# Kernel tuning notes

Measured on AMD Instinct MI355X. Metric: run time of the kernel, lower is better.

Reference implementation:

```python
import jax, jax.numpy as jnp
import numpy as np

B, T, C = 2, 2048, 2048
NH, NKV = 16, 4
HD = C // NH  # 128


def _rope(x, cos, sin):
    d = x.shape[-1] // 2
    x1, x2 = x[..., :d], x[..., d:]
    return jnp.concatenate([x1 * cos + x2 * sin, -x1 * sin + x2 * cos], axis=-1)


def _rmsnorm(x):
    eps = jnp.finfo(x.dtype).eps
    return x * jax.lax.rsqrt(jnp.mean(jnp.square(x), axis=-1, keepdims=True) + eps)


def setup_inputs() -> dict:
    key = jax.random.key(0)
    ks = jax.random.split(key, 7)
    s = 0.02
    return {
        "x": jax.random.normal(ks[0], (B, T, C), jnp.float32),
        "cos": jax.random.normal(ks[1], (1, T, 1, HD // 2), jnp.float32),
        "sin": jax.random.normal(ks[2], (1, T, 1, HD // 2), jnp.float32),
        "wq": jax.random.normal(ks[3], (C, NH * HD), jnp.float32) * s,
        "wk": jax.random.normal(ks[4], (C, NKV * HD), jnp.float32) * s,
        "wv": jax.random.normal(ks[5], (C, NKV * HD), jnp.float32) * s,
        "wo": jax.random.normal(ks[6], (C, C), jnp.float32) * s,
    }


def reference(x, cos, sin, wq, wk, wv, wo):
    q = (x @ wq).reshape(B, T, NH, HD)
    k = (x @ wk).reshape(B, T, NKV, HD)
    v = (x @ wv).reshape(B, T, NKV, HD)
    q = _rmsnorm(_rope(q, cos, sin))
    k = _rmsnorm(_rope(k, cos, sin))
    # [B, H, T, D]
    q = q.transpose(0, 2, 1, 3)
    k = k.transpose(0, 2, 1, 3)
    v = v.transpose(0, 2, 1, 3)
    rep = NH // NKV
    k = jnp.repeat(k, rep, axis=1)
    v = jnp.repeat(v, rep, axis=1)
    scale = 1.0 / jnp.sqrt(jnp.float32(HD))
    scores = jnp.einsum("bhqd,bhkd->bhqk", q, k) * scale
    causal = jnp.tril(jnp.ones((T, T), bool))
    scores = jnp.where(causal, scores, jnp.finfo(scores.dtype).min)
    attn = jax.nn.softmax(scores, axis=-1)
    y = jnp.einsum("bhqk,bhkd->bhqd", attn, v)
    y = y.transpose(0, 2, 1, 3).reshape(B, T, C)
    return y @ wo
```

## Files before the change

### kernel.cpp

```cpp
#include <hip/hip_runtime.h>
#include <hip/hip_bf16.h>
#include <cstdint>

typedef unsigned short u16;
typedef __bf16 bf16x8 __attribute__((ext_vector_type(8)));
typedef float f32x4 __attribute__((ext_vector_type(4)));
typedef unsigned short u16x4 __attribute__((ext_vector_type(4)));
typedef unsigned uint2v __attribute__((ext_vector_type(2)));

#define B_ 2
#define T_ 2048
#define C_ 2048
#define NH_ 16
#define NKV_ 4
#define HD_ 128
#define K2_ 0.12752004650581538f

__device__ __forceinline__ u16 f2bf(float f) {
    unsigned u = __builtin_bit_cast(unsigned, f);
    unsigned r = u + 0x7FFFu + ((u >> 16) & 1u);
    return (u16)(r >> 16);
}

__device__ __forceinline__ unsigned cvtpk(float a, float b) {
    unsigned r;
    asm("v_cvt_pk_bf16_f32 %0, %1, %2" : "=v"(r) : "v"(a), "v"(b));
    return r;
}

__device__ __forceinline__ void gl16(const void* g, void* l) {
    auto gp = reinterpret_cast<const __attribute__((address_space(1))) unsigned*>(
        reinterpret_cast<uintptr_t>(g));
    auto lp = reinterpret_cast<__attribute__((address_space(3))) unsigned*>(
        reinterpret_cast<uintptr_t>(l));
    __builtin_amdgcn_global_load_lds(gp, lp, 16, 0, 0);
}

__global__ void transpose_conv(const float* __restrict__ in, u16* __restrict__ out, int N) {
    __shared__ float tile[32][33];
    int n0 = blockIdx.x * 32, k0 = blockIdx.y * 32;
    int tx = threadIdx.x, ty = threadIdx.y;
#pragma unroll
    for (int i = 0; i < 4; ++i)
        tile[ty * 4 + i][tx] = in[(size_t)(k0 + ty * 4 + i) * N + n0 + tx];
    __syncthreads();
#pragma unroll
    for (int i = 0; i < 4; ++i)
        out[(size_t)(n0 + ty * 4 + i) * 2048 + k0 + tx] = f2bf(tile[tx][ty * 4 + i]);
}

__global__ void convert4(const float4* __restrict__ in, u16* __restrict__ out) {
    int i = blockIdx.x * 256 + threadIdx.x;
    float4 v = in[i];
    u16x4 o;
    o[0] = f2bf(v.x); o[1] = f2bf(v.y); o[2] = f2bf(v.z); o[3] = f2bf(v.w);
    ((u16x4*)out)[i] = o;
}

__global__ __launch_bounds__(256, 2) void gemm_bf16(const u16* __restrict__ A,
                                                    const u16* __restrict__ BT,
                                                    float* __restrict__ C, int N, int K) {
    __shared__ __align__(16) u16 As[128 * 64];
    __shared__ __align__(16) u16 Bs[128 * 64];
    int nwg = gridDim.x * gridDim.y;
    int bid = blockIdx.y * gridDim.x + blockIdx.x;
    int nb = (bid & 7) * (nwg >> 3) + (bid >> 3);
    int bx = nb % gridDim.x, by = nb / gridDim.x;

    int t = threadIdx.x;
    int w = t >> 6, l = t & 63;
    int wr = w >> 1, wc = w & 1;
    int lg = l >> 4, lr = l & 15;
    int m0 = by * 128, n0 = bx * 128;
    f32x4 acc[4][4] = {};
    int ar = t >> 3;
    int acb = (t & 7) * 16;
    const char* Abase = (const char*)(A + (size_t)(m0 + ar) * K) + acb;
    const char* Bbase = (const char*)(BT + (size_t)(n0 + ar) * K) + acb;
    char* AsB = (char*)As + t * 16;
    char* BsB = (char*)Bs + t * 16;
    for (int kt = 0; kt < K; kt += 64) {
        if (kt) __syncthreads();
#pragma unroll
        for (int i = 0; i < 4; ++i) {
            gl16(Abase + (size_t)(i * 32) * K * 2 + (size_t)kt * 2, AsB + i * 4096);
            gl16(Bbase + (size_t)(i * 32) * K * 2 + (size_t)kt * 2, BsB + i * 4096);
        }
        __syncthreads();
#pragma unroll
        for (int kk = 0; kk < 2; ++kk) {
            bf16x8 af[4], bfr[4];
#pragma unroll
            for (int m = 0; m < 4; ++m)
                af[m] = *(const bf16x8*)(As + (wr * 64 + m * 16 + lr) * 64 + kk * 32 + lg * 8);
#pragma unroll
            for (int n = 0; n < 4; ++n)
                bfr[n] = *(const bf16x8*)(Bs + (wc * 64 + n * 16 + lr) * 64 + kk * 32 + lg * 8);
#pragma unroll
            for (int m = 0; m < 4; ++m)
#pragma unroll
                for (int n = 0; n < 4; ++n)
                    acc[m][n] = __builtin_amdgcn_mfma_f32_16x16x32_bf16(af[m], bfr[n], acc[m][n], 0, 0, 0);
        }
    }
#pragma unroll
    for (int m = 0; m < 4; ++m) {
        int row = m0 + wr * 64 + m * 16 + lg * 4;
#pragma unroll
        for (int n = 0; n < 4; ++n) {
            int col = n0 + wc * 64 + n * 16 + lr;
            float* Cp = C + (size_t)row * N + col;
#pragma unroll
            for (int r = 0; r < 4; ++r)
                Cp[(size_t)r * N] = acc[m][n][r];
        }
    }
}

__global__ void rope_rms(const float* __restrict__ qkv, const float* __restrict__ cs,
                         const float* __restrict__ sn, u16* __restrict__ qh,
                         u16* __restrict__ kh) {
    int task = blockIdx.x * 4 + (threadIdx.x >> 6);
    int l = threadIdx.x & 63;
    const float* in;
    u16* out;
    int tpos;
    float post = 1.0f;
    if (task < 65536) {
        int row = task >> 4, h = task & 15;
        in = qkv + (size_t)row * 3072 + h * 128;
        int b = row >> 11; tpos = row & 2047;
        out = qh + ((size_t)(b * NH_ + h) * T_ + tpos) * HD_;
        post = K2_;
    } else {
        int t2 = task - 65536;
        int row = t2 >> 2, h = t2 & 3;
        in = qkv + (size_t)row * 3072 + 2048 + h * 128;
        int b = row >> 11; tpos = row & 2047;
        out = kh + ((size_t)(b * NKV_ + h) * T_ + tpos) * HD_;
    }
    float x1 = in[l], x2 = in[l + 64];
    float c = cs[tpos * 64 + l], s = sn[tpos * 64 + l];
    float o1 = x1 * c + x2 * s;
    float o2 = -x1 * s + x2 * c;
    float ss = o1 * o1 + o2 * o2;
#pragma unroll
    for (int m = 1; m < 64; m <<= 1) ss += __shfl_xor(ss, m);
    float r = rsqrtf(ss * (1.0f / 128.0f) + 1.1920929e-07f) * post;
    out[l] = f2bf(o1 * r);
    out[l + 64] = f2bf(o2 * r);
}

__global__ void transpose_v(const float* __restrict__ qkv, u16* __restrict__ vt) {
    __shared__ float tile[32][33];
    int t0 = blockIdx.x * 32;
    int d0 = blockIdx.y * 32;
    int bk = blockIdx.z;
    int b = bk >> 2, kvh = bk & 3;
    int tx = threadIdx.x, ty = threadIdx.y;
#pragma unroll
    for (int i = 0; i < 4; ++i)
        tile[ty * 4 + i][tx] =
            qkv[(size_t)(b * 2048 + t0 + ty * 4 + i) * 3072 + 2560 + kvh * 128 + d0 + tx];
    __syncthreads();
#pragma unroll
    for (int i = 0; i < 4; ++i)
        vt[((size_t)bk * 128 + d0 + ty * 4 + i) * 2048 + t0 + tx] = f2bf(tile[tx][ty * 4 + i]);
}

__global__ __launch_bounds__(256, 2) void attn(const u16* __restrict__ Q,
                                               const u16* __restrict__ Kk,
                                               const u16* __restrict__ V,
                                               u16* __restrict__ Y) {
    extern __shared__ __align__(16) u16 sm[];
    u16* Ks = sm;
    u16* Vs = sm + 16384;
    u16* Pb = sm + 32768;

    int bid = blockIdx.x;
    int xcd = bid & 7;
    int b = xcd >> 2, kvh = xcd & 3;
    int q = bid >> 3;
    int j = (q < 32) ? (63 - q) : (q - 32);
    int NN = (j >> 1) + 1;
    int t = threadIdx.x;
    int w = t >> 6, l = t & 63;
    int lg = l >> 4, lr = l & 15;
    int h = kvh * 4 + w;
    int qw = j * 32;

    const u16* Qp = Q + (size_t)(b * NH_ + h) * T_ * HD_;
    const u16* Kp = Kk + (size_t)(b * NKV_ + kvh) * T_ * HD_;
    const u16* Vp = V + (size_t)(b * NKV_ + kvh) * HD_ * T_;
    u16* Yp = Y + (size_t)(b * T_) * 2048 + h * HD_;
    u16* Pw = Pb + w * 2048;

    size_t koff[4], voff[4];
#pragma unroll
    for (int i = 0; i < 4; ++i) {
        int g = t + i * 256;
        koff[i] = (size_t)(g >> 4) * 256 + (size_t)(((g & 15) ^ ((g >> 4) & 15)) * 16);
        voff[i] = (size_t)(g >> 3) * (T_ * 2) + (size_t)(((g & 7) ^ ((g >> 3) & 7)) * 16);
    }
    auto stage = [&](int kv0, int buf) {
        const char* Kb = (const char*)Kp + (size_t)kv0 * 256;
        const char* Vb = (const char*)Vp + (size_t)kv0 * 2;
        char* Kd = (char*)Ks + buf * 16384 + t * 16;
        char* Vd = (char*)Vs + buf * 16384 + t * 16;
#pragma unroll
        for (int i = 0; i < 4; ++i) {
            gl16(Kb + koff[i], Kd + i * 4096);
            gl16(Vb + voff[i], Vd + i * 4096);
        }
    };

    bf16x8 aq[2][4];
#pragma unroll
    for (int qf = 0; qf < 2; ++qf)
#pragma unroll
        for (int ch = 0; ch < 4; ++ch)
            aq[qf][ch] = *(const bf16x8*)(Qp + (size_t)(qw + qf * 16 + lr) * HD_ + ch * 32 + lg * 8);

    f32x4 acc[2][8] = {};
    float m2[2] = {-1e30f, -1e30f};
    float lp_[2] = {0.0f, 0.0f};

    stage(0, 0);

    for (int gi = 0; gi < NN; ++gi) {
        asm volatile("s_waitcnt vmcnt(0)" ::: "memory");
        __builtin_amdgcn_s_barrier();
        __builtin_amdgcn_sched_barrier(0);
        int cur = gi & 1;
        if (gi + 1 < NN) stage((gi + 1) * 64, cur ^ 1);
        int kv0 = gi * 64;
        int kbase = cur * 8192;

        f32x4 sc[2][4] = {};
        __builtin_amdgcn_s_setprio(1);
#pragma unroll
        for (int ch = 0; ch < 4; ++ch)
#pragma unroll
            for (int kf = 0; kf < 4; ++kf) {
                bf16x8 bk = *(const bf16x8*)&Ks[kbase + (kf * 16 + lr) * 128 + (((ch * 4 + lg) ^ lr) * 8)];
                sc[0][kf] = __builtin_amdgcn_mfma_f32_16x16x32_bf16(bk, aq[0][ch], sc[0][kf], 0, 0, 0);
                sc[1][kf] = __builtin_amdgcn_mfma_f32_16x16x32_bf16(bk, aq[1][ch], sc[1][kf], 0, 0, 0);
            }
        __builtin_amdgcn_s_setprio(0);

        if (kv0 + 63 > qw) {
#pragma unroll
            for (int qf = 0; qf < 2; ++qf) {
                int qrow = qw + qf * 16 + lr;
#pragma unroll
                for (int kf = 0; kf < 4; ++kf)
#pragma unroll
                    for (int r = 0; r < 4; ++r) {
                        int key = kv0 + kf * 16 + 4 * lg + r;
                        if (key > qrow) sc[qf][kf][r] = -1e38f;
                    }
            }
        }
        float mx[2];
#pragma unroll
        for (int qf = 0; qf < 2; ++qf) {
            float m = sc[qf][0][0];
#pragma unroll
            for (int kf = 0; kf < 4; ++kf)
#pragma unroll
                for (int r = 0; r < 4; ++r) m = fmaxf(m, sc[qf][kf][r]);
            m = fmaxf(m, __shfl_xor(m, 16));
            m = fmaxf(m, __shfl_xor(m, 32));
            mx[qf] = m;
        }
        bool upd = (mx[0] > m2[0] + 8.0f) || (mx[1] > m2[1] + 8.0f);
        if (__any(upd)) {
#pragma unroll
            for (int qf = 0; qf < 2; ++qf) {
                float mn = fmaxf(m2[qf], mx[qf]);
                float rs = exp2f(m2[qf] - mn);
                m2[qf] = mn;
                lp_[qf] *= rs;
                float rs4[4];
#pragma unroll
                for (int r = 0; r < 4; ++r) rs4[r] = __shfl(rs, 4 * lg + r, 16);
#pragma unroll
                for (int oc = 0; oc < 8; ++oc)
#pragma unroll
                    for (int r = 0; r < 4; ++r) acc[qf][oc][r] *= rs4[r];
            }
        }
#pragma unroll
        for (int qf = 0; qf < 2; ++qf) {
            float ps = 0.0f;
#pragma unroll
            for (int kf = 0; kf < 4; ++kf) {
                float p0 = exp2f(sc[qf][kf][0] - m2[qf]);
                float p1 = exp2f(sc[qf][kf][1] - m2[qf]);
                float p2 = exp2f(sc[qf][kf][2] - m2[qf]);
                float p3 = exp2f(sc[qf][kf][3] - m2[qf]);
                ps += (p0 + p1) + (p2 + p3);
                uint2v pk;
                pk[0] = cvtpk(p0, p1);
                pk[1] = cvtpk(p2, p3);
                int g16 = 2 * kf + (lg >> 1);
                *(uint2v*)&Pw[(qf * 16 + lr) * 64 + ((g16 ^ (lr & 7)) * 8) + (lg & 1) * 4] = pk;
            }
            lp_[qf] += ps;
        }
        bf16x8 ap[2][2];
#pragma unroll
        for (int qf = 0; qf < 2; ++qf)
#pragma unroll
            for (int kk = 0; kk < 2; ++kk)
                ap[qf][kk] = *(const bf16x8*)&Pw[(qf * 16 + lr) * 64 + (((4 * kk + lg) ^ (lr & 7)) * 8)];
        __builtin_amdgcn_s_setprio(1);
#pragma unroll
        for (int oc = 0; oc < 8; ++oc)
#pragma unroll
            for (int kk = 0; kk < 2; ++kk) {
                bf16x8 bv = *(const bf16x8*)&Vs[kbase + (oc * 16 + lr) * 64 +
                                                (((kk * 4 + lg) ^ (lr & 7)) * 8)];
                acc[0][oc] = __builtin_amdgcn_mfma_f32_16x16x32_bf16(ap[0][kk], bv, acc[0][oc], 0, 0, 0);
                acc[1][oc] = __builtin_amdgcn_mfma_f32_16x16x32_bf16(ap[1][kk], bv, acc[1][oc], 0, 0, 0);
            }
        __builtin_amdgcn_s_setprio(0);
    }
#pragma unroll
    for (int qf = 0; qf < 2; ++qf) {
        float lt = lp_[qf];
        lt += __shfl_xor(lt, 16);
        lt += __shfl_xor(lt, 32);
        float inv = 1.0f / lt;
        float inv4[4];
#pragma unroll
        for (int r = 0; r < 4; ++r) inv4[r] = __shfl(inv, 4 * lg + r, 16);
#pragma unroll
        for (int oc = 0; oc < 8; ++oc)
#pragma unroll
            for (int r = 0; r < 4; ++r)
                Yp[(size_t)(qw + qf * 16 + 4 * lg + r) * 2048 + oc * 16 + lr] =
                    f2bf(acc[qf][oc][r] * inv4[r]);
    }
}

extern "C" void kernel_launch(void* const* d_in, const int* in_sizes, int n_in,
                              void* d_out, int out_size, void* d_ws, size_t ws_size,
                              hipStream_t stream) {
    const float* x    = (const float*)d_in[0];
    const float* cosT = (const float*)d_in[1];
    const float* sinT = (const float*)d_in[2];
    const float* wq   = (const float*)d_in[3];
    const float* wk   = (const float*)d_in[4];
    const float* wv   = (const float*)d_in[5];
    const float* wo   = (const float*)d_in[6];
    float* out = (float*)d_out;

    char* ws = (char*)d_ws;
    u16*   wqkvT = (u16*)(ws);
    u16*   woT   = (u16*)(ws + 12582912);
    u16*   xb    = (u16*)(ws + 20971520);
    float* qkv   = (float*)(ws + 37748736);
    u16*   qh    = (u16*)(ws + 88080384);
    u16*   kh    = (u16*)(ws + 104857600);
    u16*   vt    = (u16*)(ws + 109051904);
    u16*   y     = xb;

    hipFuncSetAttribute(reinterpret_cast<const void*>(&attn),
                        hipFuncAttributeMaxDynamicSharedMemorySize, 81920);

    transpose_conv<<<dim3(64, 64), dim3(32, 8), 0, stream>>>(wq, wqkvT, 2048);
    transpose_conv<<<dim3(16, 64), dim3(32, 8), 0, stream>>>(wk, wqkvT + (size_t)2048 * 2048, 512);
    transpose_conv<<<dim3(16, 64), dim3(32, 8), 0, stream>>>(wv, wqkvT + (size_t)2560 * 2048, 512);
    transpose_conv<<<dim3(64, 64), dim3(32, 8), 0, stream>>>(wo, woT, 2048);
    convert4<<<8192, 256, 0, stream>>>((const float4*)x, xb);

    gemm_bf16<<<dim3(24, 32), 256, 0, stream>>>(xb, wqkvT, qkv, 3072, 2048);

    rope_rms<<<20480, 256, 0, stream>>>(qkv, cosT, sinT, qh, kh);
    transpose_v<<<dim3(64, 4, 8), dim3(32, 8), 0, stream>>>(qkv, vt);

    attn<<<512, 256, 81920, stream>>>(qh, kh, vt, y);

    gemm_bf16<<<dim3(16, 32), 256, 0, stream>>>(y, woT, out, 2048, 2048);
}
```

Baseline: 224.4 us.

## Double-buffer GEMM LDS tiles with XOR swizzle and halve attention P scratch

The bf16 GEMM now stages the next K tile into a second LDS buffer while the current one feeds MFMAs, using one wait and barrier per iteration instead of two syncs. It also applies an XOR swizzle to the global-to-LDS layout to reduce bank conflicts. The attention kernel writes and reads the P tile in two 32-column halves, which halves the per-wave scratch and shrinks dynamic LDS from 81920 to 73728 bytes, possibly improving occupancy. The GEMM doubles its static LDS (64KB), which may limit it to fewer blocks per CU.

```diff
diff --git a/kernel.cpp b/kernel.cpp
--- a/kernel.cpp
+++ b/kernel.cpp
@@ -60,8 +60,8 @@
 __global__ __launch_bounds__(256, 2) void gemm_bf16(const u16* __restrict__ A,
                                                     const u16* __restrict__ BT,
                                                     float* __restrict__ C, int N, int K) {
-    __shared__ __align__(16) u16 As[128 * 64];
-    __shared__ __align__(16) u16 Bs[128 * 64];
+    __shared__ __align__(16) u16 As[2][128 * 64];
+    __shared__ __align__(16) u16 Bs[2][128 * 64];
     int nwg = gridDim.x * gridDim.y;
     int bid = blockIdx.y * gridDim.x + blockIdx.x;
     int nb = (bid & 7) * (nwg >> 3) + (bid >> 3);
@@ -73,29 +73,45 @@
     int lg = l >> 4, lr = l & 15;
     int m0 = by * 128, n0 = bx * 128;
     f32x4 acc[4][4] = {};
-    int ar = t >> 3;
-    int acb = (t & 7) * 16;
-    const char* Abase = (const char*)(A + (size_t)(m0 + ar) * K) + acb;
-    const char* Bbase = (const char*)(BT + (size_t)(n0 + ar) * K) + acb;
-    char* AsB = (char*)As + t * 16;
-    char* BsB = (char*)Bs + t * 16;
-    for (int kt = 0; kt < K; kt += 64) {
-        if (kt) __syncthreads();
+
+    size_t goff[4];
+#pragma unroll
+    for (int i = 0; i < 4; ++i) {
+        int g = t + i * 256;
+        goff[i] = (size_t)(g >> 3) * K * 2 + (size_t)(((g & 7) ^ ((g >> 3) & 7)) * 16);
+    }
+    const char* Ab = (const char*)A + (size_t)m0 * K * 2;
+    const char* Bb = (const char*)BT + (size_t)n0 * K * 2;
+
+    auto stage = [&](int kt, int buf) {
+        char* Ad = (char*)As[buf] + t * 16;
+        char* Bd = (char*)Bs[buf] + t * 16;
 #pragma unroll
         for (int i = 0; i < 4; ++i) {
-            gl16(Abase + (size_t)(i * 32) * K * 2 + (size_t)kt * 2, AsB + i * 4096);
-            gl16(Bbase + (size_t)(i * 32) * K * 2 + (size_t)kt * 2, BsB + i * 4096);
-        }
-        __syncthreads();
+            gl16(Ab + (size_t)kt * 2 + goff[i], Ad + i * 4096);
+            gl16(Bb + (size_t)kt * 2 + goff[i], Bd + i * 4096);
+        }
+    };
+
+    stage(0, 0);
+    int nk = K >> 6;
+    for (int ki = 0; ki < nk; ++ki) {
+        asm volatile("s_waitcnt vmcnt(0)" ::: "memory");
+        __builtin_amdgcn_s_barrier();
+        __builtin_amdgcn_sched_barrier(0);
+        int cur = ki & 1;
+        if (ki + 1 < nk) stage((ki + 1) * 64, cur ^ 1);
 #pragma unroll
         for (int kk = 0; kk < 2; ++kk) {
             bf16x8 af[4], bfr[4];
 #pragma unroll
             for (int m = 0; m < 4; ++m)
-                af[m] = *(const bf16x8*)(As + (wr * 64 + m * 16 + lr) * 64 + kk * 32 + lg * 8);
+                af[m] = *(const bf16x8*)&As[cur][(wr * 64 + m * 16 + lr) * 64 +
+                                                (((kk * 4 + lg) ^ (lr & 7)) * 8)];
 #pragma unroll
             for (int n = 0; n < 4; ++n)
-                bfr[n] = *(const bf16x8*)(Bs + (wc * 64 + n * 16 + lr) * 64 + kk * 32 + lg * 8);
+                bfr[n] = *(const bf16x8*)&Bs[cur][(wc * 64 + n * 16 + lr) * 64 +
+                                                 (((kk * 4 + lg) ^ (lr & 7)) * 8)];
 #pragma unroll
             for (int m = 0; m < 4; ++m)
 #pragma unroll
@@ -193,7 +209,7 @@
     const u16* Kp = Kk + (size_t)(b * NKV_ + kvh) * T_ * HD_;
     const u16* Vp = V + (size_t)(b * NKV_ + kvh) * HD_ * T_;
     u16* Yp = Y + (size_t)(b * T_) * 2048 + h * HD_;
-    u16* Pw = Pb + w * 2048;
+    u16* Pw = Pb + w * 1024;
 
     size_t koff[4], voff[4];
 #pragma unroll
@@ -290,30 +306,32 @@
                     for (int r = 0; r < 4; ++r) acc[qf][oc][r] *= rs4[r];
             }
         }
-#pragma unroll
-        for (int qf = 0; qf < 2; ++qf) {
-            float ps = 0.0f;
-#pragma unroll
-            for (int kf = 0; kf < 4; ++kf) {
-                float p0 = exp2f(sc[qf][kf][0] - m2[qf]);
-                float p1 = exp2f(sc[qf][kf][1] - m2[qf]);
-                float p2 = exp2f(sc[qf][kf][2] - m2[qf]);
-                float p3 = exp2f(sc[qf][kf][3] - m2[qf]);
-                ps += (p0 + p1) + (p2 + p3);
-                uint2v pk;
-                pk[0] = cvtpk(p0, p1);
-                pk[1] = cvtpk(p2, p3);
-                int g16 = 2 * kf + (lg >> 1);
-                *(uint2v*)&Pw[(qf * 16 + lr) * 64 + ((g16 ^ (lr & 7)) * 8) + (lg & 1) * 4] = pk;
+        bf16x8 ap[2][2];
+#pragma unroll
+        for (int kk = 0; kk < 2; ++kk) {
+#pragma unroll
+            for (int qf = 0; qf < 2; ++qf) {
+                float ps = 0.0f;
+#pragma unroll
+                for (int kfl = 0; kfl < 2; ++kfl) {
+                    int kf = kk * 2 + kfl;
+                    float p0 = exp2f(sc[qf][kf][0] - m2[qf]);
+                    float p1 = exp2f(sc[qf][kf][1] - m2[qf]);
+                    float p2 = exp2f(sc[qf][kf][2] - m2[qf]);
+                    float p3 = exp2f(sc[qf][kf][3] - m2[qf]);
+                    ps += (p0 + p1) + (p2 + p3);
+                    uint2v pk;
+                    pk[0] = cvtpk(p0, p1);
+                    pk[1] = cvtpk(p2, p3);
+                    int g = 2 * kfl + (lg >> 1);
+                    *(uint2v*)&Pw[(qf * 16 + lr) * 32 + ((g ^ (lr & 3)) * 8) + (lg & 1) * 4] = pk;
+                }
+                lp_[qf] += ps;
             }
-            lp_[qf] += ps;
-        }
-        bf16x8 ap[2][2];
-#pragma unroll
-        for (int qf = 0; qf < 2; ++qf)
-#pragma unroll
-            for (int kk = 0; kk < 2; ++kk)
-                ap[qf][kk] = *(const bf16x8*)&Pw[(qf * 16 + lr) * 64 + (((4 * kk + lg) ^ (lr & 7)) * 8)];
+#pragma unroll
+            for (int qf = 0; qf < 2; ++qf)
+                ap[qf][kk] = *(const bf16x8*)&Pw[(qf * 16 + lr) * 32 + ((lg ^ (lr & 3)) * 8)];
+        }
         __builtin_amdgcn_s_setprio(1);
 #pragma unroll
         for (int oc = 0; oc < 8; ++oc)
@@ -367,7 +385,7 @@
     u16*   y     = xb;
 
     hipFuncSetAttribute(reinterpret_cast<const void*>(&attn),
-                        hipFuncAttributeMaxDynamicSharedMemorySize, 81920);
+                        hipFuncAttributeMaxDynamicSharedMemorySize, 73728);
 
     transpose_conv<<<dim3(64, 64), dim3(32, 8), 0, stream>>>(wq, wqkvT, 2048);
     transpose_conv<<<dim3(16, 64), dim3(32, 8), 0, stream>>>(wk, wqkvT + (size_t)2048 * 2048, 512);
@@ -380,7 +398,7 @@
     rope_rms<<<20480, 256, 0, stream>>>(qkv, cosT, sinT, qh, kh);
     transpose_v<<<dim3(64, 4, 8), dim3(32, 8), 0, stream>>>(qkv, vt);
 
-    attn<<<512, 256, 81920, stream>>>(qh, kh, vt, y);
+    attn<<<512, 256, 73728, stream>>>(qh, kh, vt, y);
 
     gemm_bf16<<<dim3(16, 32), 256, 0, stream>>>(y, woT, out, 2048, 2048);
 }
```

Result: faster. 206.9 us (-7.8%).
